# Kernel optimization log

Measured on AMD Instinct MI355X. Metric: run time of the kernel, lower is better.

## Reference

```python
import jax, jax.numpy as jnp
import numpy as np


def _rot_grids(group_order, ks, dtype):
    """Normalized sampling grids for each rotation (align_corners=False convention)."""
    k = jnp.arange(group_order, dtype=dtype)
    theta = 2.0 * jnp.pi * k / group_order                      # [G]
    c, s = jnp.cos(theta), jnp.sin(theta)
    # F.affine_grid base coords with align_corners=False: centers of pixels in [-1,1]
    lin = (jnp.arange(ks, dtype=dtype) + 0.5) * (2.0 / ks) - 1.0
    y, x = jnp.meshgrid(lin, lin, indexing='ij')                 # [ks,ks] each
    # theta rows: [cos, -sin, 0], [sin, cos, 0] applied to (x, y, 1)
    gx = c[:, None, None] * x - s[:, None, None] * y             # [G,ks,ks]
    gy = s[:, None, None] * x + c[:, None, None] * y             # [G,ks,ks]
    return gx, gy


def _grid_sample_bilinear_zeros(img, gx, gy):
    """Bilinear grid_sample, padding_mode='zeros', align_corners=False.
    img: [C,H,W]; gx,gy: [G,H,W] normalized coords. Returns [C,G,H,W]."""
    C, H, W = img.shape
    dt = img.dtype
    # unnormalize (align_corners=False)
    ix = ((gx + 1.0) * W - 1.0) * 0.5
    iy = ((gy + 1.0) * H - 1.0) * 0.5
    ix0 = jnp.floor(ix)
    iy0 = jnp.floor(iy)
    wx1 = (ix - ix0).astype(dt); wx0 = 1.0 - wx1
    wy1 = (iy - iy0).astype(dt); wy0 = 1.0 - wy1

    def gather(iyf, ixf):
        xi = ixf.astype(jnp.int32)
        yi = iyf.astype(jnp.int32)
        valid = ((xi >= 0) & (xi < W) & (yi >= 0) & (yi < H)).astype(dt)
        xi_c = jnp.clip(xi, 0, W - 1)
        yi_c = jnp.clip(yi, 0, H - 1)
        return img[:, yi_c, xi_c] * valid                        # [C,G,H,W]

    out = (gather(iy0, ix0) * (wy0 * wx0)
           + gather(iy0, ix0 + 1.0) * (wy0 * wx1)
           + gather(iy0 + 1.0, ix0) * (wy1 * wx0)
           + gather(iy0 + 1.0, ix0 + 1.0) * (wy1 * wx1))
    return out


def setup_inputs() -> dict:
    key = jax.random.key(0)
    out_ch, in_ch, ks = 512, 256, 9
    base_weight = jax.random.normal(key, (out_ch, in_ch, ks, ks), dtype=jnp.float32)
    return {"base_weight": base_weight, "group_order": 8}


def reference(base_weight, group_order):
    O, I, ks, _ = base_weight.shape
    img = base_weight.reshape(O * I, ks, ks)                     # [C,H,W]
    gx, gy = _rot_grids(group_order, ks, base_weight.dtype)      # [G,ks,ks]
    out = _grid_sample_bilinear_zeros(img, gx, gy)               # [C,G,ks,ks]
    # concat over rotations along dim 0 -> [G*O, I, ks, ks]
    out = out.reshape(O, I, group_order, ks, ks).transpose(2, 0, 1, 3, 4)
    return out.reshape(group_order * O, I, ks, ks)
```

## Files before the change

### kernel.cpp

```cpp
#include <hip/hip_runtime.h>


#define KS    9
#define NPIX  81
#define NC    64
#define BLOCK 256
#define NSLOT ((NC * NPIX) / 4)

typedef float f4 __attribute__((ext_vector_type(4)));

struct Tap { int qA, qB; float w0, w1, w2, w3; };

constexpr double SQ2H = 0.70710678118654752440084436210485;
constexpr double CS[8] = {1.0,  SQ2H, 0.0, -SQ2H, -1.0, -SQ2H,  0.0,  SQ2H};
constexpr double SN[8] = {0.0,  SQ2H, 1.0,  SQ2H,  0.0, -SQ2H, -1.0, -SQ2H};

constexpr int cfloor(double v) { int i = (int)v; return (v < (double)i) ? i - 1 : i; }

constexpr Tap mk(int g, int p) {
    int py = p / KS, px = p - KS * py;
    double lx = ((double)px + 0.5) * (2.0 / KS) - 1.0;
    double ly = ((double)py + 0.5) * (2.0 / KS) - 1.0;
    double gx = CS[g] * lx - SN[g] * ly;
    double gy = SN[g] * lx + CS[g] * ly;
    double ix = ((gx + 1.0) * KS - 1.0) * 0.5;
    double iy = ((gy + 1.0) * KS - 1.0) * 0.5;
    int x0 = cfloor(ix), y0 = cfloor(iy);
    double fx = ix - x0, fy = iy - y0;
    double wx0 = 1.0 - fx, wx1 = fx;
    double pw0 = 0.0, pw1 = 0.0; int xs = 0;
    if (x0 >= 0 && x0 < KS - 1)      { xs = x0;     pw0 = wx0; pw1 = wx1; }
    else if (x0 == KS - 1)           { xs = KS - 2; pw0 = 0.0; pw1 = wx0; }
    else if (x0 == -1)               { xs = 0;      pw0 = wx1; pw1 = 0.0; }
    int yA = y0, yB = y0 + 1;
    double wyA = (yA >= 0 && yA < KS) ? (1.0 - fy) : 0.0;
    double wyB = (yB >= 0 && yB < KS) ? fy : 0.0;
    int yAc = yA < 0 ? 0 : (yA > KS - 1 ? KS - 1 : yA);
    int yBc = yB < 0 ? 0 : (yB > KS - 1 ? KS - 1 : yB);
    return Tap{ yAc * KS + xs, yBc * KS + xs,
                (float)(wyA * pw0), (float)(wyA * pw1),
                (float)(wyB * pw0), (float)(wyB * pw1) };
}

struct TapTab { Tap t[8][NPIX]; };
constexpr TapTab build_tab() {
    TapTab T{};
    for (int g = 0; g < 8; ++g)
        for (int p = 0; p < NPIX; ++p) T.t[g][p] = mk(g, p);
    return T;
}
constexpr TapTab TT = build_tab();

__device__ __forceinline__ void bar_lds() {
    __builtin_amdgcn_sched_barrier(0);
    asm volatile("s_waitcnt lgkmcnt(0)" ::: "memory");
    __builtin_amdgcn_s_barrier();
    __builtin_amdgcn_sched_barrier(0);
}

__device__ __forceinline__ void st_nt(f4* dst, f4 v) {
    __builtin_nontemporal_store(v, dst);
}

template<int G, int P>
__device__ __forceinline__ void one_out(const float (&r)[NPIX], float* otrow) {
    constexpr Tap t = TT.t[G][P];
    float v = 0.0f;
    if constexpr (t.w0 != 0.0f) v += r[t.qA]     * t.w0;
    if constexpr (t.w1 != 0.0f) v += r[t.qA + 1] * t.w1;
    if constexpr (t.w2 != 0.0f) v += r[t.qB]     * t.w2;
    if constexpr (t.w3 != 0.0f) v += r[t.qB + 1] * t.w3;
    otrow[P] = v;
}

template<int G, int P0, int NP>
__device__ __forceinline__ void compute_range(const float (&r)[NPIX], float* otrow) {
    if constexpr (NP > 0) {
        one_out<G, P0>(r, otrow);
        compute_range<G, P0 + 1, NP - 1>(r, otrow);
    }
}

template<int G>
__device__ __forceinline__ void compute_quarter(int gq, const float (&r)[NPIX],
                                                float* otrow) {
    if (gq == 0)      compute_range<G,  0, 20>(r, otrow);
    else if (gq == 1) compute_range<G, 20, 20>(r, otrow);
    else if (gq == 2) compute_range<G, 40, 20>(r, otrow);
    else              compute_range<G, 60, 21>(r, otrow);
}

__device__ __forceinline__ void cp_of(int d, int& c, int& p) {
    c = (d * 6473) >> 19;
    p = d - NPIX * c;
}

template<int G>
__device__ __forceinline__ int qe(int p) {
    if constexpr (G == 0) return p;
    else if constexpr (G == 4) return 80 - p;
    else {
        int py = (p * 57) >> 9;
        int px = p - KS * py;
        if constexpr (G == 2) return KS * px + 8 - py;
        else                  return 72 - KS * px + py;
    }
}

template<int G>
__device__ __forceinline__ void do_even(const float* lin, f4* d4, int t) {
    if constexpr (G == 0) {
        const f4* s4 = (const f4*)lin;
        for (int j = t; j < NSLOT; j += BLOCK) st_nt(&d4[j], s4[j]);
    } else {
        for (int j = t; j < NSLOT; j += BLOCK) {
            int d0 = 4 * j;
            f4 v;
#pragma unroll
            for (int k = 0; k < 4; ++k) {
                int c, p; cp_of(d0 + k, c, p);
                v[k] = lin[c * NPIX + qe<G>(p)];
            }
            st_nt(&d4[j], v);
        }
    }
}

template<int G>
__device__ __forceinline__ void do_odd(const float* lin, float* ot,
                                       f4* d4, int t) {
    const int c = t & 63, gq = t >> 6;
    float r[NPIX];
    const float* myrow = &lin[c * NPIX];
#pragma unroll
    for (int j = 0; j < NPIX; ++j) r[j] = myrow[j];
    compute_quarter<G>(gq, r, &ot[c * NPIX]);
    bar_lds();
    const f4* s4 = (const f4*)ot;
    for (int j = t; j < NSLOT; j += BLOCK) st_nt(&d4[j], s4[j]);
}

__global__ __launch_bounds__(BLOCK) void st_rotate(
        const float* __restrict__ in, float* __restrict__ out, int C) {
    __shared__ __align__(16) float lin[NC * NPIX];
    __shared__ __align__(16) float ot[NC * NPIX];
    const int t = threadIdx.x;
    const int g = blockIdx.y;
    const int c0 = blockIdx.x * NC;

    {
        const f4* src = (const f4*)(in + (size_t)c0 * NPIX);
        f4* dst = (f4*)lin;
        for (int j = t; j < NSLOT; j += BLOCK) dst[j] = src[j];
    }
    bar_lds();

    f4* d4 = (f4*)(out + ((size_t)g * C + c0) * NPIX);
    switch (g) {
        case 0: do_even<0>(lin, d4, t); break;
        case 1: do_odd <1>(lin, ot, d4, t); break;
        case 2: do_even<2>(lin, d4, t); break;
        case 3: do_odd <3>(lin, ot, d4, t); break;
        case 4: do_even<4>(lin, d4, t); break;
        case 5: do_odd <5>(lin, ot, d4, t); break;
        case 6: do_even<6>(lin, d4, t); break;
        default: do_odd<7>(lin, ot, d4, t); break;
    }
}

extern "C" void kernel_launch(void* const* d_in, const int* in_sizes, int n_in,
                              void* d_out, int out_size, void* d_ws, size_t ws_size,
                              hipStream_t stream) {
    const float* in = (const float*)d_in[0];
    float* out = (float*)d_out;
    const int C = in_sizes[0] / NPIX;
    dim3 grid(C / NC, 8, 1);
    st_rotate<<<grid, BLOCK, 0, stream>>>(in, out, C);
}
```

Measured before the change: 395.2 us.

## Process all eight rotations per block, reusing one LDS input tile

Each block now loads its 64-channel tile once and writes all eight rotations, instead of one block per rotation re-reading the input. This cuts global input reads by eightfold. Odd rotations now read taps straight from LDS rather than first copying a row into 81 registers, and nontemporal stores become ordinary stores. The trade-off is a grid with one eighth as many blocks, more serialized work and extra barriers per block, which may leave the GPU underfilled.

```diff
diff --git a/kernel.cpp b/kernel.cpp
--- a/kernel.cpp
+++ b/kernel.cpp
@@ -58,36 +58,32 @@
     __builtin_amdgcn_sched_barrier(0);
 }
 
-__device__ __forceinline__ void st_nt(f4* dst, f4 v) {
-    __builtin_nontemporal_store(v, dst);
-}
-
 template<int G, int P>
-__device__ __forceinline__ void one_out(const float (&r)[NPIX], float* otrow) {
+__device__ __forceinline__ void one_out(const float* lrow, float* otrow) {
     constexpr Tap t = TT.t[G][P];
     float v = 0.0f;
-    if constexpr (t.w0 != 0.0f) v += r[t.qA]     * t.w0;
-    if constexpr (t.w1 != 0.0f) v += r[t.qA + 1] * t.w1;
-    if constexpr (t.w2 != 0.0f) v += r[t.qB]     * t.w2;
-    if constexpr (t.w3 != 0.0f) v += r[t.qB + 1] * t.w3;
+    if constexpr (t.w0 != 0.0f) v += lrow[t.qA]     * t.w0;
+    if constexpr (t.w1 != 0.0f) v += lrow[t.qA + 1] * t.w1;
+    if constexpr (t.w2 != 0.0f) v += lrow[t.qB]     * t.w2;
+    if constexpr (t.w3 != 0.0f) v += lrow[t.qB + 1] * t.w3;
     otrow[P] = v;
 }
 
 template<int G, int P0, int NP>
-__device__ __forceinline__ void compute_range(const float (&r)[NPIX], float* otrow) {
+__device__ __forceinline__ void compute_range(const float* lrow, float* otrow) {
     if constexpr (NP > 0) {
-        one_out<G, P0>(r, otrow);
-        compute_range<G, P0 + 1, NP - 1>(r, otrow);
+        one_out<G, P0>(lrow, otrow);
+        compute_range<G, P0 + 1, NP - 1>(lrow, otrow);
     }
 }
 
 template<int G>
-__device__ __forceinline__ void compute_quarter(int gq, const float (&r)[NPIX],
+__device__ __forceinline__ void compute_quarter(int gq, const float* lrow,
                                                 float* otrow) {
-    if (gq == 0)      compute_range<G,  0, 20>(r, otrow);
-    else if (gq == 1) compute_range<G, 20, 20>(r, otrow);
-    else if (gq == 2) compute_range<G, 40, 20>(r, otrow);
-    else              compute_range<G, 60, 21>(r, otrow);
+    if (gq == 0)      compute_range<G,  0, 20>(lrow, otrow);
+    else if (gq == 1) compute_range<G, 20, 20>(lrow, otrow);
+    else if (gq == 2) compute_range<G, 40, 20>(lrow, otrow);
+    else              compute_range<G, 60, 21>(lrow, otrow);
 }
 
 __device__ __forceinline__ void cp_of(int d, int& c, int& p) {
@@ -111,7 +107,7 @@
 __device__ __forceinline__ void do_even(const float* lin, f4* d4, int t) {
     if constexpr (G == 0) {
         const f4* s4 = (const f4*)lin;
-        for (int j = t; j < NSLOT; j += BLOCK) st_nt(&d4[j], s4[j]);
+        for (int j = t; j < NSLOT; j += BLOCK) d4[j] = s4[j];
     } else {
         for (int j = t; j < NSLOT; j += BLOCK) {
             int d0 = 4 * j;
@@ -121,23 +117,14 @@
                 int c, p; cp_of(d0 + k, c, p);
                 v[k] = lin[c * NPIX + qe<G>(p)];
             }
-            st_nt(&d4[j], v);
+            d4[j] = v;
         }
     }
 }
 
-template<int G>
-__device__ __forceinline__ void do_odd(const float* lin, float* ot,
-                                       f4* d4, int t) {
-    const int c = t & 63, gq = t >> 6;
-    float r[NPIX];
-    const float* myrow = &lin[c * NPIX];
-#pragma unroll
-    for (int j = 0; j < NPIX; ++j) r[j] = myrow[j];
-    compute_quarter<G>(gq, r, &ot[c * NPIX]);
-    bar_lds();
+__device__ __forceinline__ void flush_ot(const float* ot, f4* d4, int t) {
     const f4* s4 = (const f4*)ot;
-    for (int j = t; j < NSLOT; j += BLOCK) st_nt(&d4[j], s4[j]);
+    for (int j = t; j < NSLOT; j += BLOCK) d4[j] = s4[j];
 }
 
 __global__ __launch_bounds__(BLOCK) void st_rotate(
@@ -145,7 +132,6 @@
     __shared__ __align__(16) float lin[NC * NPIX];
     __shared__ __align__(16) float ot[NC * NPIX];
     const int t = threadIdx.x;
-    const int g = blockIdx.y;
     const int c0 = blockIdx.x * NC;
 
     {
@@ -155,17 +141,33 @@
     }
     bar_lds();
 
-    f4* d4 = (f4*)(out + ((size_t)g * C + c0) * NPIX);
-    switch (g) {
-        case 0: do_even<0>(lin, d4, t); break;
-        case 1: do_odd <1>(lin, ot, d4, t); break;
-        case 2: do_even<2>(lin, d4, t); break;
-        case 3: do_odd <3>(lin, ot, d4, t); break;
-        case 4: do_even<4>(lin, d4, t); break;
-        case 5: do_odd <5>(lin, ot, d4, t); break;
-        case 6: do_even<6>(lin, d4, t); break;
-        default: do_odd<7>(lin, ot, d4, t); break;
-    }
+    f4* const ob = (f4*)(out + (size_t)c0 * NPIX);
+    const size_t gs4 = (size_t)C * NPIX / 4;
+
+    do_even<0>(lin, ob + 0 * gs4, t);
+    do_even<2>(lin, ob + 2 * gs4, t);
+    do_even<4>(lin, ob + 4 * gs4, t);
+    do_even<6>(lin, ob + 6 * gs4, t);
+
+    const int c = t & 63, gq = t >> 6;
+    const float* lrow = &lin[c * NPIX];
+    float* otrow = &ot[c * NPIX];
+
+    compute_quarter<1>(gq, lrow, otrow);
+    bar_lds();
+    flush_ot(ot, ob + 1 * gs4, t);
+    bar_lds();
+    compute_quarter<3>(gq, lrow, otrow);
+    bar_lds();
+    flush_ot(ot, ob + 3 * gs4, t);
+    bar_lds();
+    compute_quarter<5>(gq, lrow, otrow);
+    bar_lds();
+    flush_ot(ot, ob + 5 * gs4, t);
+    bar_lds();
+    compute_quarter<7>(gq, lrow, otrow);
+    bar_lds();
+    flush_ot(ot, ob + 7 * gs4, t);
 }
 
 extern "C" void kernel_launch(void* const* d_in, const int* in_sizes, int n_in,
@@ -174,6 +176,5 @@
     const float* in = (const float*)d_in[0];
     float* out = (float*)d_out;
     const int C = in_sizes[0] / NPIX;
-    dim3 grid(C / NC, 8, 1);
-    st_rotate<<<grid, BLOCK, 0, stream>>>(in, out, C);
+    st_rotate<<<C / NC, BLOCK, 0, stream>>>(in, out, C);
 }
```

Measured after the change: 365.8 us. 7.5% less time.
